# Kernel optimization log

Hardware: AMD Instinct MI355X
Metric: run time of the kernel (lower is better)

## Reference

```python
import jax, jax.numpy as jnp
import numpy as np

K = 20  # top-K neighbors per stock
SLOPE = 0.2  # LeakyReLU negative slope


def _gru_layer(x, Wih, Whh, bih, bhh):
    # x: [N, T, D]; PyTorch GRU gate order: r, z, n
    H = Whh.shape[1]
    def step(h, xt):
        gi = xt @ Wih.T + bih            # [N, 3H]
        gh = h @ Whh.T + bhh             # [N, 3H]
        ir, iz, inn = jnp.split(gi, 3, axis=1)
        hr, hz, hn = jnp.split(gh, 3, axis=1)
        r = jax.nn.sigmoid(ir + hr)
        z = jax.nn.sigmoid(iz + hz)
        n = jnp.tanh(inn + r * hn)
        h_new = (1.0 - z) * n + z * h
        return h_new, h_new
    h0 = jnp.zeros((x.shape[0], H), x.dtype)
    _, ys = jax.lax.scan(step, h0, jnp.swapaxes(x, 0, 1))
    return jnp.swapaxes(ys, 0, 1)        # [N, T, H]


def _cos_sim(x, y):
    # torch: xy / (||x|| ||y||^T), NaN (0/0) replaced by 0
    xy = x @ y.T
    xn = jnp.sqrt(jnp.sum(x * x, axis=1, keepdims=True))
    yn = jnp.sqrt(jnp.sum(y * y, axis=1, keepdims=True))
    denom = xn @ yn.T
    safe = jnp.where(denom == 0.0, 1.0, denom)
    return jnp.where(denom == 0.0, 0.0, xy / safe)


def setup_inputs() -> dict:
    key = jax.random.key(0)
    ks = jax.random.split(key, 20)
    N, T, F, H = 4096, 64, 32, 128
    def rn(k, shape, scale=0.1):
        return jax.random.normal(k, shape, dtype=jnp.float32) * scale
    b01 = lambda n: jnp.full((n,), 0.1, jnp.float32)
    return {
        'x': jax.random.normal(ks[0], (N, T, F), dtype=jnp.float32),
        'Wih0': rn(ks[1], (3 * H, F)), 'Whh0': rn(ks[2], (3 * H, H)),
        'bih0': rn(ks[3], (3 * H,)), 'bhh0': rn(ks[4], (3 * H,)),
        'Wih1': rn(ks[5], (3 * H, H)), 'Whh1': rn(ks[6], (3 * H, H)),
        'bih1': rn(ks[7], (3 * H,)), 'bhh1': rn(ks[8], (3 * H,)),
        'W_hc': rn(ks[9], (H, H)), 'b_hc': b01(H),
        'W_hs': rn(ks[10], (H, H)), 'b_hs': b01(H),
        'W_fore': rn(ks[11], (H, H)), 'b_fore': b01(H),
        'W_back': rn(ks[12], (H, H)), 'b_back': b01(H),
        'W_indi': rn(ks[13], (H, H)), 'b_indi': b01(H),
        'W_out': rn(ks[14], (1, H)), 'b_out': b01(1),
    }


def reference(x, Wih0, Whh0, bih0, bhh0, Wih1, Whh1, bih1, bhh1,
              W_hc, b_hc, W_hs, b_hs, W_fore, b_fore, W_back, b_back,
              W_indi, b_indi, W_out, b_out):
    lrelu = lambda v: jax.nn.leaky_relu(v, SLOPE)
    h = _gru_layer(x, Wih0, Whh0, bih0, bhh0)
    h = _gru_layer(h, Wih1, Whh1, bih1, bhh1)
    g = h[:, -1, :]                                   # [N, H] last-step GRU output
    N = g.shape[0]

    sim = _cos_sim(g, g)                              # [N, N]
    diag = jnp.diagonal(sim)
    sim_off = sim * (1.0 - jnp.eye(N, dtype=sim.dtype))

    # top-K (by |sim|) neighbor mask via scatter
    cols = jax.lax.top_k(jnp.abs(sim_off), K)[1]      # [N, K]
    rows = jnp.repeat(jnp.arange(N), K)
    mask = jnp.zeros((N, N), sim.dtype).at[rows, cols.reshape(-1)].set(1.0)

    tks = sim_off * mask
    col_nz = (jnp.sum(tks, axis=0) != 0).astype(sim.dtype)
    tks = tks + jnp.diag(col_nz * diag)

    # concept features; zero rows (empty concepts) are masked instead of filtered
    concept_raw = tks.T @ g                           # [N, H]
    valid = (jnp.sum(concept_raw, axis=1) != 0).astype(g.dtype)
    cf = lrelu(concept_raw @ W_hc.T + b_hc) * valid[:, None]

    attn = jax.nn.softmax(_cos_sim(g, cf), axis=0)    # softmax over stocks per concept
    hs = lrelu((attn @ cf) @ W_hs.T + b_hs)
    back = lrelu(hs @ W_back.T + b_back)
    fore = lrelu(hs @ W_fore.T + b_fore)
    indi = lrelu((g - back) @ W_indi.T + b_indi)
    pred = (fore + indi) @ W_out.T + b_out            # [N, 1]
    return pred.squeeze(-1)
```

## Files before the change

### kernel.cpp

```cpp
#include <hip/hip_runtime.h>
#include <hip/hip_bf16.h>


typedef float f32x4 __attribute__((ext_vector_type(4)));
typedef short s16x8 __attribute__((ext_vector_type(8)));
typedef unsigned short u16;
typedef unsigned long long u64;

#define DEVFN static __device__ __forceinline__

DEVFN u16 f2bf(float f) {
  union { float f; unsigned u; } v; v.f = f;
  return (u16)((v.u + 0x7FFFu + ((v.u >> 16) & 1u)) >> 16);
}

DEVFN unsigned f2bf_pk(float lo, float hi) {
  union { __hip_bfloat162 h; unsigned u; } p;
  p.h = __float22bfloat162_rn(make_float2(lo, hi));
  return p.u;
}

DEVFN f32x4 mfma16(s16x8 a, s16x8 b, f32x4 c) {
  return __builtin_amdgcn_mfma_f32_16x16x32_bf16(a, b, c, 0, 0, 0);
}
// ... 94 lines not shown
#pragma unroll
    for (int i = 0; i < 4; i += 2) {
      float hn[2];
#pragma unroll
      for (int q = 0; q < 2; ++q) {
        int ii = i + q;
        float rr = sigmf(ai[0][ii] + brz0[0]);
        float zg = sigmf(ai[1][ii] + brz0[1]);
        float nn = tanhf_fast(ai[2][ii] + bin0 + rr * bhn0);
        hn[q] = nn - zg * nn;
        h0reg[ii] = hn[q];
      }
      unsigned pk = f2bf_pk(hn[0], hn[1]);
      int m = quad * 4 + i;
      sh_h0[0][m * 136 + c]       = (u16)pk;
      sh_h0[0][(m + 1) * 136 + c] = (u16)(pk >> 16);
    }
  }

#define GRU_STEP(T, CUR, NXT)                                                     \
  {                                                                               \
    __syncthreads();                                                              \
    s16x8 ah0[4], ah1[4];                                                         \
    _Pragma("unroll")                                                             \
    for (int kk = 0; kk < 4; ++kk) {                                              \
      ah0[kk] = *(const s16x8*)(sh_h0[CUR] + l16 * 136 + kk * 32 + quad * 8);     \
      ah1[kk] = *(const s16x8*)(sh_h1[CUR] + l16 * 136 + kk * 32 + quad * 8);     \
    }                                                                             \
    s16x8 ax = *(const s16x8*)(sh_x[(T) + 1] + l16 * 40 + quad * 8);              \
    f32x4 r1a, z1a, ni1, nh1, r0a, z0a, ni0, nh0;                                 \
    r1a = mfma16(ah0[0], B1ih[0][0], zz4);                                        \
    z1a = mfma16(ah0[0], B1ih[1][0], zz4);                                        \
    ni1 = mfma16(ah0[0], B1ih[2][0], zz4);                                        \
    nh1 = mfma16(ah1[0], B1hh[2][0], zz4);                                        \
    r0a = mfma16(ax, B0ih[0], zz4);                                               \
    z0a = mfma16(ax, B0ih[1], zz4);                                               \
    ni0 = mfma16(ax, B0ih[2], zz4);                                               \
    nh0 = mfma16(ah0[0], B0hh[2][0], zz4);                                        \
    _Pragma("unroll")                                                             \
    for (int kk = 1; kk < 4; ++kk) {                                              \
      r1a = mfma16(ah0[kk], B1ih[0][kk], r1a);                                    \
      z1a = mfma16(ah0[kk], B1ih[1][kk], z1a);                                    \
      ni1 = mfma16(ah0[kk], B1ih[2][kk], ni1);                                    \
      nh1 = mfma16(ah1[kk], B1hh[2][kk], nh1);                                    \
      nh0 = mfma16(ah0[kk], B0hh[2][kk], nh0);                                    \
    }                                                                             \
    _Pragma("unroll")                                                             \
    for (int kk = 0; kk < 4; ++kk) {                                              \
      r1a = mfma16(ah1[kk], B1hh[0][kk], r1a);                                    \
      z1a = mfma16(ah1[kk], B1hh[1][kk], z1a);                                    \
      r0a = mfma16(ah0[kk], B0hh[0][kk], r0a);                                    \
      z0a = mfma16(ah0[kk], B0hh[1][kk], z0a);                                    \
    }                                                                             \
    _Pragma("unroll")                                                             \
    for (int i = 0; i < 4; i += 2) {                                              \
      float hn[2];                                                                \
      _Pragma("unroll")                                                           \
      for (int q = 0; q < 2; ++q) {                                               \
        int ii = i + q;                                                           \
        float rr = sigmf(r1a[ii] + brz1[0]);                                      \
        float zg = sigmf(z1a[ii] + brz1[1]);                                      \
        float nn = tanhf_fast(ni1[ii] + bin1 + rr * (nh1[ii] + bhn1));            \
        hn[q] = nn + zg * (h1reg[ii] - nn);                                       \
        h1reg[ii] = hn[q];                                                        \
      }                                                                           \
      unsigned pk = f2bf_pk(hn[0], hn[1]);                                        \
      int m = quad * 4 + i;                                                       \
      sh_h1[NXT][m * 136 + c]       = (u16)pk;                                    \
      sh_h1[NXT][(m + 1) * 136 + c] = (u16)(pk >> 16);                            \
    }                                                                             \
    _Pragma("unroll")                                                             \
    for (int i = 0; i < 4; i += 2) {                                              \
      float hn[2];                                                                \
      _Pragma("unroll")                                                           \
      for (int q = 0; q < 2; ++q) {                                               \
        int ii = i + q;                                                           \
        float rr = sigmf(r0a[ii] + brz0[0]);                                      \
        float zg = sigmf(z0a[ii] + brz0[1]);                                      \
        float nn = tanhf_fast(ni0[ii] + bin0 + rr * (nh0[ii] + bhn0));            \
        hn[q] = nn + zg * (h0reg[ii] - nn);                                       \
        h0reg[ii] = hn[q];                                                        \
      }                                                                           \
      unsigned pk = f2bf_pk(hn[0], hn[1]);                                        \
      int m = quad * 4 + i;                                                       \
      sh_h0[NXT][m * 136 + c]       = (u16)pk;                                    \
      sh_h0[NXT][(m + 1) * 136 + c] = (u16)(pk >> 16);                            \
    }                                                                             \
  }

  for (int t2 = 0; t2 < 31; ++t2) {
    int t = t2 * 2;
    GRU_STEP(t, 0, 1);
    GRU_STEP(t + 1, 1, 0);
  }
  GRU_STEP(62, 0, 1);
#undef GRU_STEP

  __syncthreads();
  {
    s16x8 ah0[4], ah1[4];
#pragma unroll
    for (int kk = 0; kk < 4; ++kk) {
      ah0[kk] = *(const s16x8*)(sh_h0[1] + l16 * 136 + kk * 32 + quad * 8);
      ah1[kk] = *(const s16x8*)(sh_h1[1] + l16 * 136 + kk * 32 + quad * 8);
    }
    f32x4 r1a, z1a, ni1, nh1;
    r1a = mfma16(ah0[0], B1ih[0][0], zz4);
    z1a = mfma16(ah0[0], B1ih[1][0], zz4);
    ni1 = mfma16(ah0[0], B1ih[2][0], zz4);
    nh1 = mfma16(ah1[0], B1hh[2][0], zz4);
#pragma unroll
    for (int kk = 1; kk < 4; ++kk) {
      r1a = mfma16(ah0[kk], B1ih[0][kk], r1a);
      z1a = mfma16(ah0[kk], B1ih[1][kk], z1a);
      ni1 = mfma16(ah0[kk], B1ih[2][kk], ni1);
      nh1 = mfma16(ah1[kk], B1hh[2][kk], nh1);
    }
#pragma unroll
    for (int kk = 0; kk < 4; ++kk) {
      r1a = mfma16(ah1[kk], B1hh[0][kk], r1a);
      z1a = mfma16(ah1[kk], B1hh[1][kk], z1a);
    }
    float hv[4];
#pragma unroll
    for (int i = 0; i < 4; ++i) {
      int m = quad * 4 + i;
      float rr = sigmf(r1a[i] + brz1[0]);
      float zg = sigmf(z1a[i] + brz1[1]);
      float nn = tanhf_fast(ni1[i] + bin1 + rr * (nh1[i] + bhn1));
      float hnew = nn + zg * (h1reg[i] - nn);
      hv[i] = hnew;
      g_out[(size_t)(r0 + m) * 128 + c] = hnew;
      gbf[(size_t)(r0 + m) * 128 + c]   = f2bf(hnew);
    }
#pragma unroll
    for (int i = 0; i < 4; ++i) {
      float s = hv[i] * hv[i];
      s += __shfl_xor(s, 1);
      s += __shfl_xor(s, 2);
      s += __shfl_xor(s, 4);
      s += __shfl_xor(s, 8);
      if (l16 == 0) red16[quad * 4 + i][w] = s;
    }
  }
  __syncthreads();
  if (tid < 16) {
    float s = 0.f;
#pragma unroll
    for (int k = 0; k < 8; ++k) s += red16[tid][k];
    rn[r0 + tid] = (s == 0.f) ? 0.f : rsqrtf(s);
  }
}

template<int MODE>
__launch_bounds__(256, 1)
__global__ void cos_gemm(const u16* __restrict__ A, const u16* __restrict__ B,
                         const float* __restrict__ rnA, const float* __restrict__ rnB,
                         float* __restrict__ C, u16* __restrict__ E,
                         float* __restrict__ colsum)
{
  __shared__ u16 shA[128 * 136];
  __shared__ u16 shB[128 * 136];
  const int tid = threadIdx.x;
  const int l = tid & 63, wv = tid >> 6;
  const int quad = l >> 4, l16 = l & 15;
  const int i0 = blockIdx.y * 128, j0 = blockIdx.x * 128;
  {
    int r = tid >> 1, half = tid & 1;
    const int4* sa = (const int4*)(A + (size_t)(i0 + r) * 128 + half * 64);
    int4* da = (int4*)(shA + r * 136 + half * 64);
    const int4* sb = (const int4*)(B + (size_t)(j0 + r) * 128 + half * 64);
    int4* db = (int4*)(shB + r * 136 + half * 64);
#pragma unroll
    for (int q = 0; q < 8; ++q) { da[q] = sa[q]; db[q] = sb[q]; }
  }
  __syncthreads();
  const int wm = wv >> 1, wn = wv & 1;
  f32x4 acc[4][4];
  const f32x4 zz4 = {0.f, 0.f, 0.f, 0.f};
#pragma unroll
  for (int a = 0; a < 4; ++a)
#pragma unroll
    for (int b = 0; b < 4; ++b) acc[a][b] = zz4;
#pragma unroll
  for (int kk = 0; kk < 4; ++kk) {
    s16x8 af[4], bfr[4];
#pragma unroll
    for (int mt = 0; mt < 4; ++mt)
      af[mt] = *(const s16x8*)(shA + (wm * 64 + mt * 16 + l16) * 136 + kk * 32 + quad * 8);
#pragma unroll
    for (int nt = 0; nt < 4; ++nt)
      bfr[nt] = *(const s16x8*)(shB + (wn * 64 + nt * 16 + l16) * 136 + kk * 32 + quad * 8);
#pragma unroll
    for (int mt = 0; mt < 4; ++mt)
#pragma unroll
      for (int nt = 0; nt < 4; ++nt) acc[mt][nt] = mfma16(af[mt], bfr[nt], acc[mt][nt]);
  }
  float ra[4][4];
#pragma unroll
  for (int mt = 0; mt < 4; ++mt)
#pragma unroll
    for (int i = 0; i < 4; ++i) ra[mt][i] = rnA[i0 + wm * 64 + mt * 16 + quad * 4 + i];
#pragma unroll
  for (int nt = 0; nt < 4; ++nt) {
    int col = j0 + wn * 64 + nt * 16 + l16;
    float rb = rnB[col];
    float psum = 0.f;
#pragma unroll
    for (int mt = 0; mt < 4; ++mt)
#pragma unroll
      for (int i = 0; i < 4; ++i) {
        int row = i0 + wm * 64 + mt * 16 + quad * 4 + i;
        float v = acc[mt][nt][i] * ra[mt][i] * rb;
        if constexpr (MODE == 0) {
          C[(size_t)row * 4096 + col] = v;
        } else {
          float e = __expf(v);
          E[(size_t)row * 4096 + col] = f2bf(e);
          psum += e;
        }
      }
    if constexpr (MODE == 1) {
      psum += __shfl_xor(psum, 16);
      psum += __shfl_xor(psum, 32);
      if (quad == 0) atomicAdd(colsum + col, psum);
    }
  }
}

__launch_bounds__(256, 1)
__global__ void topk_select(const float* __restrict__ sim,
                            int* __restrict__ gselj, float* __restrict__ gselv,
                            int* __restrict__ cnt, int* __restrict__ touched)
{
  __shared__ unsigned hist[2048];
  __shared__ u64 cand[3072];
  __shared__ int selj[20];
  __shared__ unsigned ws4[4];
  __shared__ unsigned wmin4[4], wmax4[4];
  __shared__ int shb, shcnt;
  const int tid = threadIdx.x;
  const int row = blockIdx.x;
  const int l = tid & 63, wv = tid >> 6;

  for (int i = tid; i < 2048; i += 256) hist[i] = 0;
  if (tid == 0) shcnt = 0;

  unsigned key[4][4];
  unsigned lmin = 0xFFFFFFFFu, lmax = 0u;
#pragma unroll
  for (int q = 0; q < 4; ++q) {
    int e0 = (q * 256 + tid) * 4;
    float4 v = *(const float4*)(sim + (size_t)row * 4096 + e0);
    key[q][0] = (e0 + 0 == row) ? 0u : (__float_as_uint(v.x) & 0x7FFFFFFFu);
    key[q][1] = (e0 + 1 == row) ? 0u : (__float_as_uint(v.y) & 0x7FFFFFFFu);
    key[q][2] = (e0 + 2 == row) ? 0u : (__float_as_uint(v.z) & 0x7FFFFFFFu);
    key[q][3] = (e0 + 3 == row) ? 0u : (__float_as_uint(v.w) & 0x7FFFFFFFu);
#pragma unroll
    for (int c = 0; c < 4; ++c) {
      unsigned k = key[q][c];
      lmin = k < lmin ? k : lmin;
      lmax = k > lmax ? k : lmax;
    }
  }
#pragma unroll
  for (int off = 1; off < 64; off <<= 1) {
    unsigned om = __shfl_xor(lmin, off); lmin = om < lmin ? om : lmin;
    unsigned ox = __shfl_xor(lmax, off); lmax = ox > lmax ? ox : lmax;
  }
  if (l == 0) { wmin4[wv] = lmin; wmax4[wv] = lmax; }
  __syncthreads();
  const unsigned kmin = min(min(wmin4[0], wmin4[1]), min(wmin4[2], wmin4[3]));
  const unsigned kmax = max(max(wmax4[0], wmax4[1]), max(wmax4[2], wmax4[3]));
  const float binscale = (kmax > kmin) ? (2047.0f / (float)(kmax - kmin)) : 0.0f;

#define BIN_OF(k) ((int)((float)((k) - kmin) * binscale))

#pragma unroll
  for (int q = 0; q < 4; ++q)
#pragma unroll
    for (int c = 0; c < 4; ++c) {
      int bin = BIN_OF(key[q][c]); if (bin > 2047) bin = 2047;
      atomicAdd(&hist[bin], 1u);
    }
  __syncthreads();

  unsigned s = 0;
#pragma unroll
  for (int j = 0; j < 8; ++j) s += hist[tid * 8 + j];
  unsigned r = s;
#pragma unroll
  for (int off = 1; off < 64; off <<= 1) {
    unsigned o = __shfl_down(r, off);
    if (l + off < 64) r += o;
  }
  if (l == 0) ws4[wv] = r;
  __syncthreads();
  unsigned upper = 0;
  for (int q = wv + 1; q < 4; ++q) upper += ws4[q];
  unsigned excl = upper + (r - s);
  if (excl < 20u && excl + s >= 20u) {
    unsigned cum = excl;
    for (int j = 7; j >= 0; --j) {
      cum += hist[tid * 8 + j];
      if (cum >= 20u) { shb = tid * 8 + j; break; }
    }
  }
  __syncthreads();
  const int b = shb;

#pragma unroll
  for (int q = 0; q < 4; ++q) {
    int e0 = (q * 256 + tid) * 4;
#pragma unroll
    for (int c = 0; c < 4; ++c) {
      int bin = BIN_OF(key[q][c]); if (bin > 2047) bin = 2047;
      if (bin >= b) {
        int p = atomicAdd(&shcnt, 1);
        if (p < 3072) cand[p] = ((u64)key[q][c] << 32) | (u64)(4095 - (e0 + c));
      }
    }
  }
#undef BIN_OF
  __syncthreads();
  const int C = (shcnt < 3072) ? shcnt : 3072;

  if (wv == 0) {
    if (C <= 64) {
      u64 mykey = (l < C) ? cand[l] : 0ull;
      for (int it = 0; it < 20; ++it) {
        u64 m = mykey;
#pragma unroll
        for (int off = 1; off < 64; off <<= 1) {
          u64 o = __shfl_xor(m, off);
          if (o > m) m = o;
        }
        if (mykey == m) mykey = 0ull;
        if (l == 0) selj[it] = 4095 - (int)(m & 0xFFFull);
      }
    } else {
      for (int it = 0; it < 20; ++it) {
        u64 best = 0ull; int bpos = -1;
        for (int p = l; p < C; p += 64) {
          u64 cv = cand[p];
          if (cv > best) { best = cv; bpos = p; }
        }
        u64 mine = best;
#pragma unroll
        for (int off = 1; off < 64; off <<= 1) {
          u64 o = __shfl_xor(best, off);
          if (o > best) best = o;
        }
        if (mine == best && bpos >= 0 && best != 0ull) cand[bpos] = 0ull;
        if (l == 0) selj[it] = 4095 - (int)(best & 0xFFFull);
      }
    }
  }
  __syncthreads();
  if (tid < 20) {
    int idx = selj[tid];
    float sv = (idx == row) ? 0.f : sim[(size_t)row * 4096 + idx];
    gselj[row * 20 + tid] = idx;
    gselv[row * 20 + tid] = sv;
    atomicAdd(&cnt[idx], 1);
    if (sv != 0.f) atomicOr(touched + idx, 1);
  }
}

__launch_bounds__(1024, 1)
__global__ void scan4096(const int* __restrict__ cnt, int* __restrict__ offs,
                         int* __restrict__ cur)
{
  __shared__ int wsum[16];
  const int t = threadIdx.x, l = t & 63, wv = t >> 6;
  int4 c = ((const int4*)cnt)[t];
  int s = c.x + c.y + c.z + c.w;
  int ps = s;
#pragma unroll
  for (int off = 1; off < 64; off <<= 1) {
    int o = __shfl_up(ps, off);
    if (l >= off) ps += o;
  }
  if (l == 63) wsum[wv] = ps;
  __syncthreads();
  if (t == 0) {
    int a = 0;
#pragma unroll
    for (int q = 0; q < 16; ++q) { int x = wsum[q]; wsum[q] = a; a += x; }
  }
  __syncthreads();
  int base = wsum[wv] + (ps - s);
  int4 o4;
  o4.x = base; o4.y = o4.x + c.x; o4.z = o4.y + c.y; o4.w = o4.z + c.z;
  ((int4*)offs)[t] = o4;
  ((int4*)cur)[t] = o4;
}

__global__ void scatter_entries(const int* __restrict__ gselj, const float* __restrict__ gselv,
                                int* __restrict__ cur, int* __restrict__ eid,
                                float* __restrict__ ev)
{
  unsigned idx = blockIdx.x * 256 + threadIdx.x;
  unsigned row = idx / 20u;
  int j = gselj[idx]; float v = gselv[idx];
  int pos = atomicAdd(&cur[j], 1);
  eid[pos] = (int)row; ev[pos] = v;
}

__launch_bounds__(128, 1)
__global__ void concept_cf(const int* __restrict__ offs, const int* __restrict__ cnt,
                           const int* __restrict__ eid, const float* __restrict__ ev,
                           const float* __restrict__ g, const float* __restrict__ rng,
                           const int* __restrict__ touched,
                           const float* __restrict__ Whc, const float* __restrict__ bhc,
                           float* __restrict__ cf, u16* __restrict__ cfbf,
                           float* __restrict__ rncf)
{
  __shared__ float shc[128];
  __shared__ float red2[2];
  const int j = blockIdx.x, d = threadIdx.x;
  const int l = d & 63, wv = d >> 6;
  const int off = offs[j], n = cnt[j];
  float acc = 0.f;
  for (int p = 0; p < n; ++p) {
    int i = eid[off + p]; float v = ev[off + p];
    acc += v * g[(size_t)i * 128 + d];
  }
  if (touched[j] && rng[j] != 0.f) acc += g[(size_t)j * 128 + d];
  float s = acc;
#pragma unroll
  for (int o = 32; o >= 1; o >>= 1) s += __shfl_xor(s, o);
  if (l == 0) red2[wv] = s;
  shc[d] = acc;
  __syncthreads();
  float valid = ((red2[0] + red2[1]) != 0.f) ? 1.f : 0.f;
  float o = bhc[d];
  const float4* wr = (const float4*)(Whc + (size_t)d * 128);
#pragma unroll 8
  for (int q = 0; q < 32; ++q) {
    float4 w4 = wr[q];
    float4 c4 = *((const float4*)shc + q);
    o += c4.x * w4.x + c4.y * w4.y + c4.z * w4.z + c4.w * w4.w;
  }
  float cfv = lrelu(o) * valid;
  cf[(size_t)j * 128 + d] = cfv;
  cfbf[(size_t)j * 128 + d] = f2bf(cfv);
  __syncthreads();
  float nn = cfv * cfv;
#pragma unroll
  for (int of = 32; of >= 1; of >>= 1) nn += __shfl_xor(nn, of);
  if (l == 0) red2[wv] = nn;
  __syncthreads();
  if (d == 0) {
    float q2 = red2[0] + red2[1];
    rncf[j] = (q2 == 0.f) ? 0.f : rsqrtf(q2);
  }
}

__launch_bounds__(256, 1)
__global__ void scale_cfT(const float* __restrict__ cf, const float* __restrict__ colsum,
                          u16* __restrict__ cfTs)
{
  __shared__ float tile[32][132];
  __shared__ float rz[32];
  const int t = threadIdx.x;
  const int c0 = blockIdx.x * 32;
  if (t < 32) rz[t] = __builtin_amdgcn_rcpf(colsum[c0 + t]);
#pragma unroll
  for (int k = 0; k < 4; ++k) {
    int lin = k * 256 + t;
    int r = lin >> 5;
    int q = lin & 31;
    float4 v = *(const float4*)(cf + (size_t)(c0 + r) * 128 + q * 4);
    tile[r][q * 4 + 0] = v.x; tile[r][q * 4 + 1] = v.y;
    tile[r][q * 4 + 2] = v.z; tile[r][q * 4 + 3] = v.w;
  }
  __syncthreads();
#pragma unroll
  for (int k = 0; k < 4; ++k) {
    int lin = k * 256 + t;
    int n  = lin >> 3;
    int c4 = (lin & 7) * 4;
    ushort4 o;
    o.x = f2bf(tile[c4 + 0][n] * rz[c4 + 0]);
    o.y = f2bf(tile[c4 + 1][n] * rz[c4 + 1]);
    o.z = f2bf(tile[c4 + 2][n] * rz[c4 + 2]);
    o.w = f2bf(tile[c4 + 3][n] * rz[c4 + 3]);
    *(ushort4*)(cfTs + (size_t)n * 4096 + c0 + c4) = o;
  }
}

__launch_bounds__(256, 1)
__global__ void attn_cf(const u16* __restrict__ attn, const u16* __restrict__ cfT,
                        float* __restrict__ hs_pre)
{
  __shared__ u16 shw[16 * 136];
  const int tid = threadIdx.x;
  const int l = tid & 63, wv = tid >> 6;
  const int quad = l >> 4, l16 = l & 15;
  const int r0 = blockIdx.x * 16;
  f32x4 acc[2];
  const f32x4 zz4 = {0.f, 0.f, 0.f, 0.f};
  acc[0] = zz4; acc[1] = zz4;
  for (int kc = 0; kc < 32; ++kc) {
    if (kc) __syncthreads();
    {
      int r = tid >> 4, seg = tid & 15;
      *(int4*)(shw + r * 136 + seg * 8) =
        *(const int4*)(attn + (size_t)(r0 + r) * 4096 + kc * 128 + seg * 8);
    }
    __syncthreads();
#pragma unroll
    for (int kk = 0; kk < 4; ++kk) {
      s16x8 a = *(const s16x8*)(shw + l16 * 136 + kk * 32 + quad * 8);
#pragma unroll
      for (int nt = 0; nt < 2; ++nt) {
        int n = wv * 32 + nt * 16 + l16;
        s16x8 b = *(const s16x8*)(cfT + (size_t)n * 4096 + kc * 128 + kk * 32 + quad * 8);
        acc[nt] = mfma16(a, b, acc[nt]);
      }
    }
  }
#pragma unroll
  for (int nt = 0; nt < 2; ++nt)
#pragma unroll
    for (int i = 0; i < 4; ++i) {
      int row = r0 + quad * 4 + i;
      int col = wv * 32 + nt * 16 + l16;
      hs_pre[(size_t)row * 128 + col] = acc[nt][i];
    }
}

__launch_bounds__(256, 1)
__global__ void head_kernel(const float* __restrict__ hs_pre, const float* __restrict__ g,
                            const u16* __restrict__ whs, const u16* __restrict__ wfore,
                            const u16* __restrict__ wback, const u16* __restrict__ windi,
                            const float* __restrict__ b_hs, const float* __restrict__ b_fore,
                            const float* __restrict__ b_back, const float* __restrict__ b_indi,
                            const float* __restrict__ W_out, const float* __restrict__ b_out,
                            float* __restrict__ outp)
{
  __shared__ u16 bufin[16 * 136];
  __shared__ u16 bufB[16 * 136];
  __shared__ float bufF[16 * 132];
  __shared__ float shWout[128];
  const int tid = threadIdx.x;
  const int l = tid & 63, wv = tid >> 6;
  const int quad = l >> 4, l16 = l & 15;
  const int r0 = blockIdx.x * 16;
  const f32x4 zz4 = {0.f, 0.f, 0.f, 0.f};

  if (tid < 128) shWout[tid] = W_out[tid];
  for (int idx = tid; idx < 2048; idx += 256) {
    int j = idx >> 7, n = idx & 127;
    bufin[j * 136 + n] = f2bf(hs_pre[(size_t)(r0 + j) * 128 + n]);
  }
  __syncthreads();
  {
    s16x8 a[4];
#pragma unroll
    for (int kk = 0; kk < 4; ++kk)
      a[kk] = *(const s16x8*)(bufin + l16 * 136 + kk * 32 + quad * 8);
    f32x4 acc[2]; acc[0] = zz4; acc[1] = zz4;
#pragma unroll
    for (int nt = 0; nt < 2; ++nt) {
      int n = wv * 32 + nt * 16 + l16;
#pragma unroll
      for (int kk = 0; kk < 4; ++kk)
        acc[nt] = mfma16(a[kk], *(const s16x8*)(whs + n * 128 + kk * 32 + quad * 8), acc[nt]);
    }
#pragma unroll
    for (int nt = 0; nt < 2; ++nt) {
      int n = wv * 32 + nt * 16 + l16;
      float bb = b_hs[n];
#pragma unroll
      for (int i = 0; i < 4; ++i)
        bufB[(quad * 4 + i) * 136 + n] = f2bf(lrelu(acc[nt][i] + bb));
    }
  }
  __syncthreads();
  {
    s16x8 a[4];
#pragma unroll
    for (int kk = 0; kk < 4; ++kk)
      a[kk] = *(const s16x8*)(bufB + l16 * 136 + kk * 32 + quad * 8);
    f32x4 aF[2], aB[2]; aF[0] = zz4; aF[1] = zz4; aB[0] = zz4; aB[1] = zz4;
#pragma unroll
    for (int nt = 0; nt < 2; ++nt) {
      int n = wv * 32 + nt * 16 + l16;
#pragma unroll
      for (int kk = 0; kk < 4; ++kk) {
        aF[nt] = mfma16(a[kk], *(const s16x8*)(wfore + n * 128 + kk * 32 + quad * 8), aF[nt]);
        aB[nt] = mfma16(a[kk], *(const s16x8*)(wback + n * 128 + kk * 32 + quad * 8), aB[nt]);
      }
    }
#pragma unroll
    for (int nt = 0; nt < 2; ++nt) {
      int n = wv * 32 + nt * 16 + l16;
      float bf_ = b_fore[n], bb_ = b_back[n];
#pragma unroll
      for (int i = 0; i < 4; ++i) {
        int m = quad * 4 + i;
        bufF[m * 132 + n] = lrelu(aF[nt][i] + bf_);
        float back = lrelu(aB[nt][i] + bb_);
        float gv = g[(size_t)(r0 + m) * 128 + n];
        bufin[m * 136 + n] = f2bf(gv - back);
      }
    }
  }
  __syncthreads();
  {
    s16x8 a[4];
#pragma unroll
    for (int kk = 0; kk < 4; ++kk)
      a[kk] = *(const s16x8*)(bufin + l16 * 136 + kk * 32 + quad * 8);
    f32x4 acc[2]; acc[0] = zz4; acc[1] = zz4;
#pragma unroll
    for (int nt = 0; nt < 2; ++nt) {
      int n = wv * 32 + nt * 16 + l16;
#pragma unroll
      for (int kk = 0; kk < 4; ++kk)
        acc[nt] = mfma16(a[kk], *(const s16x8*)(windi + n * 128 + kk * 32 + quad * 8), acc[nt]);
    }
#pragma unroll
    for (int nt = 0; nt < 2; ++nt) {
      int n = wv * 32 + nt * 16 + l16;
      float bi_ = b_indi[n];
#pragma unroll
      for (int i = 0; i < 4; ++i)
        bufF[(quad * 4 + i) * 132 + n] += lrelu(acc[nt][i] + bi_);
    }
  }
  __syncthreads();
  if (tid < 16) {
    float s = b_out[0];
    const float* fr = bufF + tid * 132;
    for (int n = 0; n < 128; ++n) s += fr[n] * shWout[n];
    outp[r0 + tid] = s;
  }
}

static const size_t OFF_A       = 0;
static const size_t OFF_ATTN    = 67108864;
static const size_t OFF_G       = 100663296;
static const size_t OFF_GBF     = 102760448;
static const size_t OFF_RNG     = 103809024;
static const size_t OFF_SELJ    = 103825408;
static const size_t OFF_SELV    = 104153088;
static const size_t OFF_EID     = 104480768;
static const size_t OFF_EV      = 104808448;
static const size_t OFF_CNT     = 105136128;
static const size_t OFF_TOUCH   = 105152512;
static const size_t OFF_COLSUM  = 105168896;
static const size_t OFF_OFFS    = 105185280;
static const size_t OFF_CUR     = 105201664;
static const size_t OFF_CF      = 105218048;
static const size_t OFF_CFBF    = 107315200;
static const size_t OFF_CFTS    = 108363776;
static const size_t OFF_RNCF    = 109412352;
static const size_t OFF_HSPRE   = 109428736;
static const size_t OFF_WB      = 111525888;

extern "C" void kernel_launch(void* const* d_in, const int* in_sizes, int n_in,
                              void* d_out, int out_size, void* d_ws, size_t ws_size,
                              hipStream_t stream)
{
  (void)in_sizes; (void)n_in; (void)out_size; (void)ws_size;
  const float* x      = (const float*)d_in[0];
  const float* Wih0   = (const float*)d_in[1];
  const float* Whh0   = (const float*)d_in[2];
  const float* bih0   = (const float*)d_in[3];
  const float* bhh0   = (const float*)d_in[4];
  const float* Wih1   = (const float*)d_in[5];
  const float* Whh1   = (const float*)d_in[6];
  const float* bih1   = (const float*)d_in[7];
  const float* bhh1   = (const float*)d_in[8];
  const float* W_hc   = (const float*)d_in[9];
  const float* b_hc   = (const float*)d_in[10];
  const float* W_hs   = (const float*)d_in[11];
  const float* b_hs   = (const float*)d_in[12];
  const float* W_fore = (const float*)d_in[13];
  const float* b_fore = (const float*)d_in[14];
  const float* W_back = (const float*)d_in[15];
  const float* b_back = (const float*)d_in[16];
  const float* W_indi = (const float*)d_in[17];
  const float* b_indi = (const float*)d_in[18];
  const float* W_out  = (const float*)d_in[19];
  const float* b_out  = (const float*)d_in[20];

  char* ws = (char*)d_ws;
  float* simbuf  = (float*)(ws + OFF_A);
  u16*   attnb   = (u16*)(ws + OFF_ATTN);
  float* gbuf    = (float*)(ws + OFF_G);
  u16*   gbf     = (u16*)(ws + OFF_GBF);
  float* rng     = (float*)(ws + OFF_RNG);
  int*   gselj   = (int*)(ws + OFF_SELJ);
  float* gselv   = (float*)(ws + OFF_SELV);
  int*   eid     = (int*)(ws + OFF_EID);
  float* ev      = (float*)(ws + OFF_EV);
  int*   cntb    = (int*)(ws + OFF_CNT);
  int*   touched = (int*)(ws + OFF_TOUCH);
  float* colsum  = (float*)(ws + OFF_COLSUM);
  int*   offsb   = (int*)(ws + OFF_OFFS);
  int*   curb    = (int*)(ws + OFF_CUR);
  float* cf      = (float*)(ws + OFF_CF);
  u16*   cfbf    = (u16*)(ws + OFF_CFBF);
  u16*   cfTs    = (u16*)(ws + OFF_CFTS);
  float* rncf    = (float*)(ws + OFF_RNCF);
  float* hs_pre  = (float*)(ws + OFF_HSPRE);
  u16*   wsB     = (u16*)(ws + OFF_WB);
  u16 *wih0b = wsB, *whh0b = wsB + 12288, *wih1b = wsB + 61440, *whh1b = wsB + 110592;
  u16 *whsb = wsB + 159744, *wforeb = wsB + 176128, *wbackb = wsB + 192512, *windib = wsB + 208896;

  cvt_all<<<880, 256, 0, stream>>>(Wih0, Whh0, Wih1, Whh1, W_hs, W_fore, W_back, W_indi,
                                   wsB, cntb);

  gru_fused<<<256, 512, 0, stream>>>(x, wih0b, whh0b, bih0, bhh0,
                                     wih1b, whh1b, bih1, bhh1, gbuf, gbf, rng);

  cos_gemm<0><<<dim3(32, 32), 256, 0, stream>>>(gbf, gbf, rng, rng, simbuf,
                                                (u16*)nullptr, (float*)nullptr);

  topk_select<<<4096, 256, 0, stream>>>(simbuf, gselj, gselv, cntb, touched);
  scan4096<<<1, 1024, 0, stream>>>(cntb, offsb, curb);
  scatter_entries<<<320, 256, 0, stream>>>(gselj, gselv, curb, eid, ev);
  concept_cf<<<4096, 128, 0, stream>>>(offsb, cntb, eid, ev, gbuf, rng, touched,
                                       W_hc, b_hc, cf, cfbf, rncf);

  cos_gemm<1><<<dim3(32, 32), 256, 0, stream>>>(gbf, cfbf, rng, rncf, (float*)nullptr,
                                                attnb, colsum);
  scale_cfT<<<128, 256, 0, stream>>>(cf, colsum, cfTs);
  attn_cf<<<256, 256, 0, stream>>>(attnb, cfTs, hs_pre);

  head_kernel<<<256, 256, 0, stream>>>(hs_pre, gbuf, whsb, wforeb, wbackb, windib,
                                       b_hs, b_fore, b_back, b_indi, W_out, b_out,
                                       (float*)d_out);
}
```

Before: 429.3 us.

## Fuse similarity GEMM into top-k and recompute attention instead of materializing NxN

Replaces the materialized 4096x4096 fp32 similarity matrix and its separate top-k pass with a fused kernel that computes 16-row similarity tiles with MFMA three times (min/max, histogram, candidate collection), never writing the matrix to memory. Likewise the bf16 exp-attention matrix is no longer stored: one GEMM only accumulates column sums, and the attention-times-cf kernel recomputes exp(cos) per tile in shared memory. This removes roughly 100MB of global traffic at the cost of redundant matrix-core recompute and a 512-bin histogram per row instead of 2048 bins, which may produce more candidates.

```diff
diff --git a/kernel.cpp b/kernel.cpp
--- a/kernel.cpp
+++ b/kernel.cpp
@@ -270,12 +270,272 @@
   }
 }
 
-template<int MODE>
+__launch_bounds__(512, 1)
+__global__ void sim_topk(const u16* __restrict__ A, const float* __restrict__ rn,
+                         int* __restrict__ gselj, float* __restrict__ gselv,
+                         int* __restrict__ cnt, int* __restrict__ touched)
+{
+  __shared__ unsigned hist[16][512];
+  __shared__ u64 cand[16][256];
+  __shared__ unsigned kmn[16], kmx[16];
+  __shared__ int cnt16[16], bthr[16];
+  const int tid = threadIdx.x;
+  const int w = tid >> 6, l = tid & 63;
+  const int quad = l >> 4, l16 = l & 15;
+  const int r0 = blockIdx.x * 16;
+  const f32x4 zz4 = {0.f, 0.f, 0.f, 0.f};
+
+  for (int i = tid; i < 16 * 512; i += 512) (&hist[0][0])[i] = 0u;
+  if (tid < 16) { kmn[tid] = 0xFFFFFFFFu; kmx[tid] = 0u; cnt16[tid] = 0; }
+
+  s16x8 af[4];
+#pragma unroll
+  for (int kk = 0; kk < 4; ++kk)
+    af[kk] = *(const s16x8*)(A + (size_t)(r0 + l16) * 128 + kk * 32 + quad * 8);
+  float ra[4];
+#pragma unroll
+  for (int i = 0; i < 4; ++i) ra[i] = rn[r0 + quad * 4 + i];
+  __syncthreads();
+
+#define SIM_TILE(T, BODY)                                                       \
+  {                                                                             \
+    int col = (T) * 128 + w * 16 + l16;                                         \
+    s16x8 bf[4];                                                                \
+    _Pragma("unroll")                                                           \
+    for (int kk = 0; kk < 4; ++kk)                                              \
+      bf[kk] = *(const s16x8*)(A + (size_t)col * 128 + kk * 32 + quad * 8);     \
+    f32x4 acc = zz4;                                                            \
+    _Pragma("unroll")                                                           \
+    for (int kk = 0; kk < 4; ++kk) acc = mfma16(af[kk], bf[kk], acc);           \
+    float rb = rn[col];                                                         \
+    _Pragma("unroll")                                                           \
+    for (int i = 0; i < 4; ++i) {                                               \
+      float v = acc[i] * ra[i] * rb;                                            \
+      unsigned kv = (col == r0 + quad * 4 + i)                                  \
+                        ? 0u : (__float_as_uint(v) & 0x7FFFFFFFu);              \
+      BODY                                                                      \
+    }                                                                           \
+  }
+
+  unsigned lmn[4] = {0xFFFFFFFFu, 0xFFFFFFFFu, 0xFFFFFFFFu, 0xFFFFFFFFu};
+  unsigned lmx[4] = {0u, 0u, 0u, 0u};
+  for (int t = 0; t < 32; ++t)
+    SIM_TILE(t, { (void)v;
+      lmn[i] = kv < lmn[i] ? kv : lmn[i];
+      lmx[i] = kv > lmx[i] ? kv : lmx[i]; })
+#pragma unroll
+  for (int i = 0; i < 4; ++i) {
+#pragma unroll
+    for (int off = 1; off < 16; off <<= 1) {
+      unsigned om = __shfl_xor(lmn[i], off); lmn[i] = om < lmn[i] ? om : lmn[i];
+      unsigned ox = __shfl_xor(lmx[i], off); lmx[i] = ox > lmx[i] ? ox : lmx[i];
+    }
+    if (l16 == 0) {
+      atomicMin(&kmn[quad * 4 + i], lmn[i]);
+      atomicMax(&kmx[quad * 4 + i], lmx[i]);
+    }
+  }
+  __syncthreads();
+  unsigned kb[4]; float scl[4];
+#pragma unroll
+  for (int i = 0; i < 4; ++i) {
+    unsigned mn = kmn[quad * 4 + i], mx = kmx[quad * 4 + i];
+    kb[i] = mn;
+    scl[i] = (mx > mn) ? (511.0f / (float)(mx - mn)) : 0.0f;
+  }
+
+  for (int t = 0; t < 32; ++t)
+    SIM_TILE(t, { (void)v;
+      int bin = (int)((float)(kv - kb[i]) * scl[i]); if (bin > 511) bin = 511;
+      atomicAdd(&hist[quad * 4 + i][bin], 1u); })
+  __syncthreads();
+
+  for (int rr = 0; rr < 2; ++rr) {
+    int row = w * 2 + rr;
+    unsigned s = 0;
+#pragma unroll
+    for (int j = 0; j < 8; ++j) s += hist[row][l * 8 + j];
+    unsigned r = s;
+#pragma unroll
+    for (int off = 1; off < 64; off <<= 1) {
+      unsigned o = __shfl_down(r, off);
+      if (l + off < 64) r += o;
+    }
+    unsigned excl = r - s;
+    if (excl < 20u && excl + s >= 20u) {
+      unsigned cum = excl;
+      for (int j = 7; j >= 0; --j) {
+        cum += hist[row][l * 8 + j];
+        if (cum >= 20u) { bthr[row] = l * 8 + j; break; }
+      }
+    }
+  }
+  __syncthreads();
+  int bth[4];
+#pragma unroll
+  for (int i = 0; i < 4; ++i) bth[i] = bthr[quad * 4 + i];
+
+  for (int t = 0; t < 32; ++t)
+    SIM_TILE(t, {
+      int bin = (int)((float)(kv - kb[i]) * scl[i]); if (bin > 511) bin = 511;
+      if (bin >= bth[i]) {
+        int p = atomicAdd(&cnt16[quad * 4 + i], 1);
+        if (p < 256) {
+          unsigned sgn = kv ? (__float_as_uint(v) >> 31) : 0u;
+          cand[quad * 4 + i][p] =
+              ((u64)kv << 13) | ((u64)(4095 - col) << 1) | (u64)sgn;
+        }
+      }
+    })
+#undef SIM_TILE
+  __syncthreads();
+
+  for (int rr = 0; rr < 2; ++rr) {
+    int row = w * 2 + rr;
+    int C = cnt16[row] < 256 ? cnt16[row] : 256;
+    int grow = r0 + row;
+    if (C <= 64) {
+      u64 my = (l < C) ? cand[row][l] : 0ull;
+      for (int it = 0; it < 20; ++it) {
+        u64 m = my;
+#pragma unroll
+        for (int off = 1; off < 64; off <<= 1) {
+          u64 o = __shfl_xor(m, off);
+          if (o > m) m = o;
+        }
+        if (my == m) my = 0ull;
+        if (l == 0) {
+          int idx = 4095 - (int)((m >> 1) & 0xFFFull);
+          unsigned kv = (unsigned)(m >> 13);
+          float sv = kv ? __uint_as_float(((unsigned)(m & 1) << 31) | kv) : 0.0f;
+          gselj[grow * 20 + it] = idx;
+          gselv[grow * 20 + it] = sv;
+          atomicAdd(&cnt[idx], 1);
+          if (sv != 0.f) atomicOr(touched + idx, 1);
+        }
+      }
+    } else {
+      for (int it = 0; it < 20; ++it) {
+        u64 best = 0ull; int bpos = -1;
+        for (int p = l; p < C; p += 64) {
+          u64 cv = cand[row][p];
+          if (cv > best) { best = cv; bpos = p; }
+        }
+        u64 mine = best;
+#pragma unroll
+        for (int off = 1; off < 64; off <<= 1) {
+          u64 o = __shfl_xor(best, off);
+          if (o > best) best = o;
+        }
+        if (mine == best && bpos >= 0 && best != 0ull) cand[row][bpos] = 0ull;
+        if (l == 0) {
+          int idx = 4095 - (int)((best >> 1) & 0xFFFull);
+          unsigned kv = (unsigned)(best >> 13);
+          float sv = kv ? __uint_as_float(((unsigned)(best & 1) << 31) | kv) : 0.0f;
+          gselj[grow * 20 + it] = idx;
+          gselv[grow * 20 + it] = sv;
+          atomicAdd(&cnt[idx], 1);
+          if (sv != 0.f) atomicOr(touched + idx, 1);
+        }
+      }
+    }
+  }
+}
+
+__launch_bounds__(1024, 1)
+__global__ void scan4096(const int* __restrict__ cnt, int* __restrict__ offs,
+                         int* __restrict__ cur)
+{
+  __shared__ int wsum[16];
+  const int t = threadIdx.x, l = t & 63, wv = t >> 6;
+  int4 c = ((const int4*)cnt)[t];
+  int s = c.x + c.y + c.z + c.w;
+  int ps = s;
+#pragma unroll
+  for (int off = 1; off < 64; off <<= 1) {
+    int o = __shfl_up(ps, off);
+    if (l >= off) ps += o;
+  }
+  if (l == 63) wsum[wv] = ps;
+  __syncthreads();
+  if (t == 0) {
+    int a = 0;
+#pragma unroll
+    for (int q = 0; q < 16; ++q) { int x = wsum[q]; wsum[q] = a; a += x; }
+  }
+  __syncthreads();
+  int base = wsum[wv] + (ps - s);
+  int4 o4;
+  o4.x = base; o4.y = o4.x + c.x; o4.z = o4.y + c.y; o4.w = o4.z + c.z;
+  ((int4*)offs)[t] = o4;
+  ((int4*)cur)[t] = o4;
+}
+
+__global__ void scatter_entries(const int* __restrict__ gselj, const float* __restrict__ gselv,
+                                int* __restrict__ cur, int* __restrict__ eid,
+                                float* __restrict__ ev)
+{
+  unsigned idx = blockIdx.x * 256 + threadIdx.x;
+  unsigned row = idx / 20u;
+  int j = gselj[idx]; float v = gselv[idx];
+  int pos = atomicAdd(&cur[j], 1);
+  eid[pos] = (int)row; ev[pos] = v;
+}
+
+__launch_bounds__(128, 1)
+__global__ void concept_cf(const int* __restrict__ offs, const int* __restrict__ cnt,
+                           const int* __restrict__ eid, const float* __restrict__ ev,
+                           const float* __restrict__ g, const float* __restrict__ rng,
+                           const int* __restrict__ touched,
+                           const float* __restrict__ Whc, const float* __restrict__ bhc,
+                           float* __restrict__ cf, u16* __restrict__ cfbf,
+                           float* __restrict__ rncf)
+{
+  __shared__ float shc[128];
+  __shared__ float red2[2];
+  const int j = blockIdx.x, d = threadIdx.x;
+  const int l = d & 63, wv = d >> 6;
+  const int off = offs[j], n = cnt[j];
+  float acc = 0.f;
+  for (int p = 0; p < n; ++p) {
+    int i = eid[off + p]; float v = ev[off + p];
+    acc += v * g[(size_t)i * 128 + d];
+  }
+  if (touched[j] && rng[j] != 0.f) acc += g[(size_t)j * 128 + d];
+  float s = acc;
+#pragma unroll
+  for (int o = 32; o >= 1; o >>= 1) s += __shfl_xor(s, o);
+  if (l == 0) red2[wv] = s;
+  shc[d] = acc;
+  __syncthreads();
+  float valid = ((red2[0] + red2[1]) != 0.f) ? 1.f : 0.f;
+  float o = bhc[d];
+  const float4* wr = (const float4*)(Whc + (size_t)d * 128);
+#pragma unroll 8
+  for (int q = 0; q < 32; ++q) {
+    float4 w4 = wr[q];
+    float4 c4 = *((const float4*)shc + q);
+    o += c4.x * w4.x + c4.y * w4.y + c4.z * w4.z + c4.w * w4.w;
+  }
+  float cfv = lrelu(o) * valid;
+  cf[(size_t)j * 128 + d] = cfv;
+  cfbf[(size_t)j * 128 + d] = f2bf(cfv);
+  __syncthreads();
+  float nn = cfv * cfv;
+#pragma unroll
+  for (int of = 32; of >= 1; of >>= 1) nn += __shfl_xor(nn, of);
+  if (l == 0) red2[wv] = nn;
+  __syncthreads();
+  if (d == 0) {
+    float q2 = red2[0] + red2[1];
+    rncf[j] = (q2 == 0.f) ? 0.f : rsqrtf(q2);
+  }
+}
+
 __launch_bounds__(256, 1)
-__global__ void cos_gemm(const u16* __restrict__ A, const u16* __restrict__ B,
-                         const float* __restrict__ rnA, const float* __restrict__ rnB,
-                         float* __restrict__ C, u16* __restrict__ E,
-                         float* __restrict__ colsum)
+__global__ void colsum_gemm(const u16* __restrict__ A, const u16* __restrict__ B,
+                            const float* __restrict__ rnA, const float* __restrict__ rnB,
+                            float* __restrict__ colsum)
 {
   __shared__ u16 shA[128 * 136];
   __shared__ u16 shB[128 * 136];
@@ -328,250 +588,12 @@
     for (int mt = 0; mt < 4; ++mt)
 #pragma unroll
       for (int i = 0; i < 4; ++i) {
-        int row = i0 + wm * 64 + mt * 16 + quad * 4 + i;
         float v = acc[mt][nt][i] * ra[mt][i] * rb;
-        if constexpr (MODE == 0) {
-          C[(size_t)row * 4096 + col] = v;
-        } else {
-          float e = __expf(v);
-          E[(size_t)row * 4096 + col] = f2bf(e);
-          psum += e;
-        }
-      }
-    if constexpr (MODE == 1) {
-      psum += __shfl_xor(psum, 16);
-      psum += __shfl_xor(psum, 32);
-      if (quad == 0) atomicAdd(colsum + col, psum);
-    }
-  }
-}
-
-__launch_bounds__(256, 1)
-__global__ void topk_select(const float* __restrict__ sim,
-                            int* __restrict__ gselj, float* __restrict__ gselv,
-                            int* __restrict__ cnt, int* __restrict__ touched)
-{
-  __shared__ unsigned hist[2048];
-  __shared__ u64 cand[3072];
-  __shared__ int selj[20];
-  __shared__ unsigned ws4[4];
-  __shared__ unsigned wmin4[4], wmax4[4];
-  __shared__ int shb, shcnt;
-  const int tid = threadIdx.x;
-  const int row = blockIdx.x;
-  const int l = tid & 63, wv = tid >> 6;
-
-  for (int i = tid; i < 2048; i += 256) hist[i] = 0;
-  if (tid == 0) shcnt = 0;
-
-  unsigned key[4][4];
-  unsigned lmin = 0xFFFFFFFFu, lmax = 0u;
-#pragma unroll
-  for (int q = 0; q < 4; ++q) {
-    int e0 = (q * 256 + tid) * 4;
-    float4 v = *(const float4*)(sim + (size_t)row * 4096 + e0);
-    key[q][0] = (e0 + 0 == row) ? 0u : (__float_as_uint(v.x) & 0x7FFFFFFFu);
-    key[q][1] = (e0 + 1 == row) ? 0u : (__float_as_uint(v.y) & 0x7FFFFFFFu);
-    key[q][2] = (e0 + 2 == row) ? 0u : (__float_as_uint(v.z) & 0x7FFFFFFFu);
-    key[q][3] = (e0 + 3 == row) ? 0u : (__float_as_uint(v.w) & 0x7FFFFFFFu);
-#pragma unroll
-    for (int c = 0; c < 4; ++c) {
-      unsigned k = key[q][c];
-      lmin = k < lmin ? k : lmin;
-      lmax = k > lmax ? k : lmax;
-    }
-  }
-#pragma unroll
-  for (int off = 1; off < 64; off <<= 1) {
-    unsigned om = __shfl_xor(lmin, off); lmin = om < lmin ? om : lmin;
-    unsigned ox = __shfl_xor(lmax, off); lmax = ox > lmax ? ox : lmax;
-  }
-  if (l == 0) { wmin4[wv] = lmin; wmax4[wv] = lmax; }
-  __syncthreads();
-  const unsigned kmin = min(min(wmin4[0], wmin4[1]), min(wmin4[2], wmin4[3]));
-  const unsigned kmax = max(max(wmax4[0], wmax4[1]), max(wmax4[2], wmax4[3]));
-  const float binscale = (kmax > kmin) ? (2047.0f / (float)(kmax - kmin)) : 0.0f;
-
-#define BIN_OF(k) ((int)((float)((k) - kmin) * binscale))
-
-#pragma unroll
-  for (int q = 0; q < 4; ++q)
-#pragma unroll
-    for (int c = 0; c < 4; ++c) {
-      int bin = BIN_OF(key[q][c]); if (bin > 2047) bin = 2047;
-      atomicAdd(&hist[bin], 1u);
-    }
-  __syncthreads();
-
-  unsigned s = 0;
-#pragma unroll
-  for (int j = 0; j < 8; ++j) s += hist[tid * 8 + j];
-  unsigned r = s;
-#pragma unroll
-  for (int off = 1; off < 64; off <<= 1) {
-    unsigned o = __shfl_down(r, off);
-    if (l + off < 64) r += o;
-  }
-  if (l == 0) ws4[wv] = r;
-  __syncthreads();
-  unsigned upper = 0;
-  for (int q = wv + 1; q < 4; ++q) upper += ws4[q];
-  unsigned excl = upper + (r - s);
-  if (excl < 20u && excl + s >= 20u) {
-    unsigned cum = excl;
-    for (int j = 7; j >= 0; --j) {
-      cum += hist[tid * 8 + j];
-      if (cum >= 20u) { shb = tid * 8 + j; break; }
-    }
-  }
-  __syncthreads();
-  const int b = shb;
-
-#pragma unroll
-  for (int q = 0; q < 4; ++q) {
-    int e0 = (q * 256 + tid) * 4;
-#pragma unroll
-    for (int c = 0; c < 4; ++c) {
-      int bin = BIN_OF(key[q][c]); if (bin > 2047) bin = 2047;
-      if (bin >= b) {
-        int p = atomicAdd(&shcnt, 1);
-        if (p < 3072) cand[p] = ((u64)key[q][c] << 32) | (u64)(4095 - (e0 + c));
-      }
-    }
-  }
-#undef BIN_OF
-  __syncthreads();
-  const int C = (shcnt < 3072) ? shcnt : 3072;
-
-  if (wv == 0) {
-    if (C <= 64) {
-      u64 mykey = (l < C) ? cand[l] : 0ull;
-      for (int it = 0; it < 20; ++it) {
-        u64 m = mykey;
-#pragma unroll
-        for (int off = 1; off < 64; off <<= 1) {
-          u64 o = __shfl_xor(m, off);
-          if (o > m) m = o;
-        }
-        if (mykey == m) mykey = 0ull;
-        if (l == 0) selj[it] = 4095 - (int)(m & 0xFFFull);
-      }
-    } else {
-      for (int it = 0; it < 20; ++it) {
-        u64 best = 0ull; int bpos = -1;
-        for (int p = l; p < C; p += 64) {
-          u64 cv = cand[p];
-          if (cv > best) { best = cv; bpos = p; }
-        }
-        u64 mine = best;
-#pragma unroll
-        for (int off = 1; off < 64; off <<= 1) {
-          u64 o = __shfl_xor(best, off);
-          if (o > best) best = o;
-        }
-        if (mine == best && bpos >= 0 && best != 0ull) cand[bpos] = 0ull;
-        if (l == 0) selj[it] = 4095 - (int)(best & 0xFFFull);
-      }
-    }
-  }
-  __syncthreads();
-  if (tid < 20) {
-    int idx = selj[tid];
-    float sv = (idx == row) ? 0.f : sim[(size_t)row * 4096 + idx];
-    gselj[row * 20 + tid] = idx;
-    gselv[row * 20 + tid] = sv;
-    atomicAdd(&cnt[idx], 1);
-    if (sv != 0.f) atomicOr(touched + idx, 1);
-  }
-}
-
-__launch_bounds__(1024, 1)
-__global__ void scan4096(const int* __restrict__ cnt, int* __restrict__ offs,
-                         int* __restrict__ cur)
-{
-  __shared__ int wsum[16];
-  const int t = threadIdx.x, l = t & 63, wv = t >> 6;
-  int4 c = ((const int4*)cnt)[t];
-  int s = c.x + c.y + c.z + c.w;
-  int ps = s;
-#pragma unroll
-  for (int off = 1; off < 64; off <<= 1) {
-    int o = __shfl_up(ps, off);
-    if (l >= off) ps += o;
-  }
-  if (l == 63) wsum[wv] = ps;
-  __syncthreads();
-  if (t == 0) {
-    int a = 0;
-#pragma unroll
-    for (int q = 0; q < 16; ++q) { int x = wsum[q]; wsum[q] = a; a += x; }
-  }
-  __syncthreads();
-  int base = wsum[wv] + (ps - s);
-  int4 o4;
-  o4.x = base; o4.y = o4.x + c.x; o4.z = o4.y + c.y; o4.w = o4.z + c.z;
-  ((int4*)offs)[t] = o4;
-  ((int4*)cur)[t] = o4;
-}
-
-__global__ void scatter_entries(const int* __restrict__ gselj, const float* __restrict__ gselv,
-                                int* __restrict__ cur, int* __restrict__ eid,
-                                float* __restrict__ ev)
-{
-  unsigned idx = blockIdx.x * 256 + threadIdx.x;
-  unsigned row = idx / 20u;
-  int j = gselj[idx]; float v = gselv[idx];
-  int pos = atomicAdd(&cur[j], 1);
-  eid[pos] = (int)row; ev[pos] = v;
-}
-
-__launch_bounds__(128, 1)
-__global__ void concept_cf(const int* __restrict__ offs, const int* __restrict__ cnt,
-                           const int* __restrict__ eid, const float* __restrict__ ev,
-                           const float* __restrict__ g, const float* __restrict__ rng,
-                           const int* __restrict__ touched,
-                           const float* __restrict__ Whc, const float* __restrict__ bhc,
-                           float* __restrict__ cf, u16* __restrict__ cfbf,
-                           float* __restrict__ rncf)
-{
-  __shared__ float shc[128];
-  __shared__ float red2[2];
-  const int j = blockIdx.x, d = threadIdx.x;
-  const int l = d & 63, wv = d >> 6;
-  const int off = offs[j], n = cnt[j];
-  float acc = 0.f;
-  for (int p = 0; p < n; ++p) {
-    int i = eid[off + p]; float v = ev[off + p];
-    acc += v * g[(size_t)i * 128 + d];
-  }
-  if (touched[j] && rng[j] != 0.f) acc += g[(size_t)j * 128 + d];
-  float s = acc;
-#pragma unroll
-  for (int o = 32; o >= 1; o >>= 1) s += __shfl_xor(s, o);
-  if (l == 0) red2[wv] = s;
-  shc[d] = acc;
-  __syncthreads();
-  float valid = ((red2[0] + red2[1]) != 0.f) ? 1.f : 0.f;
-  float o = bhc[d];
-  const float4* wr = (const float4*)(Whc + (size_t)d * 128);
-#pragma unroll 8
-  for (int q = 0; q < 32; ++q) {
-    float4 w4 = wr[q];
-    float4 c4 = *((const float4*)shc + q);
-    o += c4.x * w4.x + c4.y * w4.y + c4.z * w4.z + c4.w * w4.w;
-  }
-  float cfv = lrelu(o) * valid;
-  cf[(size_t)j * 128 + d] = cfv;
-  cfbf[(size_t)j * 128 + d] = f2bf(cfv);
-  __syncthreads();
-  float nn = cfv * cfv;
-#pragma unroll
-  for (int of = 32; of >= 1; of >>= 1) nn += __shfl_xor(nn, of);
-  if (l == 0) red2[wv] = nn;
-  __syncthreads();
-  if (d == 0) {
-    float q2 = red2[0] + red2[1];
-    rncf[j] = (q2 == 0.f) ? 0.f : rsqrtf(q2);
+        psum += __expf(v);
+      }
+    psum += __shfl_xor(psum, 16);
+    psum += __shfl_xor(psum, 32);
+    if (quad == 0) atomicAdd(colsum + col, psum);
   }
 }
 
@@ -609,32 +631,57 @@
 }
 
 __launch_bounds__(256, 1)
-__global__ void attn_cf(const u16* __restrict__ attn, const u16* __restrict__ cfT,
-                        float* __restrict__ hs_pre)
-{
-  __shared__ u16 shw[16 * 136];
+__global__ void attn_fused(const u16* __restrict__ gbf, const float* __restrict__ rng,
+                           const u16* __restrict__ cfbf, const float* __restrict__ rncf,
+                           const u16* __restrict__ cfT, float* __restrict__ hs_pre)
+{
+  __shared__ u16 shE[16 * 136];
   const int tid = threadIdx.x;
   const int l = tid & 63, wv = tid >> 6;
   const int quad = l >> 4, l16 = l & 15;
   const int r0 = blockIdx.x * 16;
-  f32x4 acc[2];
   const f32x4 zz4 = {0.f, 0.f, 0.f, 0.f};
-  acc[0] = zz4; acc[1] = zz4;
-  for (int kc = 0; kc < 32; ++kc) {
-    if (kc) __syncthreads();
-    {
-      int r = tid >> 4, seg = tid & 15;
-      *(int4*)(shw + r * 136 + seg * 8) =
-        *(const int4*)(attn + (size_t)(r0 + r) * 4096 + kc * 128 + seg * 8);
+
+  s16x8 ag[4];
+#pragma unroll
+  for (int kk = 0; kk < 4; ++kk)
+    ag[kk] = *(const s16x8*)(gbf + (size_t)(r0 + l16) * 128 + kk * 32 + quad * 8);
+  float ra[4];
+#pragma unroll
+  for (int i = 0; i < 4; ++i) ra[i] = rng[r0 + quad * 4 + i];
+
+  f32x4 acc[2]; acc[0] = zz4; acc[1] = zz4;
+  for (int ct = 0; ct < 32; ++ct) {
+    int c0 = ct * 128;
+    f32x4 a2[2]; a2[0] = zz4; a2[1] = zz4;
+#pragma unroll
+    for (int nt = 0; nt < 2; ++nt) {
+      int cc = c0 + wv * 32 + nt * 16 + l16;
+#pragma unroll
+      for (int kk = 0; kk < 4; ++kk) {
+        s16x8 b = *(const s16x8*)(cfbf + (size_t)cc * 128 + kk * 32 + quad * 8);
+        a2[nt] = mfma16(ag[kk], b, a2[nt]);
+      }
+    }
+    if (ct) __syncthreads();
+#pragma unroll
+    for (int nt = 0; nt < 2; ++nt) {
+      int cl = wv * 32 + nt * 16 + l16;
+      float rb = rncf[c0 + cl];
+#pragma unroll
+      for (int i = 0; i < 4; ++i) {
+        float e = __expf(a2[nt][i] * ra[i] * rb);
+        shE[(quad * 4 + i) * 136 + cl] = f2bf(e);
+      }
     }
     __syncthreads();
 #pragma unroll
     for (int kk = 0; kk < 4; ++kk) {
-      s16x8 a = *(const s16x8*)(shw + l16 * 136 + kk * 32 + quad * 8);
+      s16x8 a = *(const s16x8*)(shE + l16 * 136 + kk * 32 + quad * 8);
 #pragma unroll
       for (int nt = 0; nt < 2; ++nt) {
         int n = wv * 32 + nt * 16 + l16;
-        s16x8 b = *(const s16x8*)(cfT + (size_t)n * 4096 + kc * 128 + kk * 32 + quad * 8);
+        s16x8 b = *(const s16x8*)(cfT + (size_t)n * 4096 + c0 + kk * 32 + quad * 8);
         acc[nt] = mfma16(a, b, acc[nt]);
       }
     }
@@ -758,26 +805,24 @@
   }
 }
 
-static const size_t OFF_A       = 0;
-static const size_t OFF_ATTN    = 67108864;
-static const size_t OFF_G       = 100663296;
-static const size_t OFF_GBF     = 102760448;
-static const size_t OFF_RNG     = 103809024;
-static const size_t OFF_SELJ    = 103825408;
-static const size_t OFF_SELV    = 104153088;
-static const size_t OFF_EID     = 104480768;
-static const size_t OFF_EV      = 104808448;
-static const size_t OFF_CNT     = 105136128;
-static const size_t OFF_TOUCH   = 105152512;
-static const size_t OFF_COLSUM  = 105168896;
-static const size_t OFF_OFFS    = 105185280;
-static const size_t OFF_CUR     = 105201664;
-static const size_t OFF_CF      = 105218048;
-static const size_t OFF_CFBF    = 107315200;
-static const size_t OFF_CFTS    = 108363776;
-static const size_t OFF_RNCF    = 109412352;
-static const size_t OFF_HSPRE   = 109428736;
-static const size_t OFF_WB      = 111525888;
+static const size_t OFF_G      = 0;
+static const size_t OFF_GBF    = 2097152;
+static const size_t OFF_RNG    = 3145728;
+static const size_t OFF_SELJ   = 3162112;
+static const size_t OFF_SELV   = 3489792;
+static const size_t OFF_EID    = 3817472;
+static const size_t OFF_EV     = 4145152;
+static const size_t OFF_CNT    = 4472832;
+static const size_t OFF_TOUCH  = 4489216;
+static const size_t OFF_COLSUM = 4505600;
+static const size_t OFF_OFFS   = 4521984;
+static const size_t OFF_CUR    = 4538368;
+static const size_t OFF_CF     = 4554752;
+static const size_t OFF_CFBF   = 6651904;
+static const size_t OFF_CFTS   = 7700480;
+static const size_t OFF_RNCF   = 8749056;
+static const size_t OFF_HSPRE  = 8765440;
+static const size_t OFF_WB     = 10862592;
 
 extern "C" void kernel_launch(void* const* d_in, const int* in_sizes, int n_in,
                               void* d_out, int out_size, void* d_ws, size_t ws_size,
@@ -807,8 +852,6 @@
   const float* b_out  = (const float*)d_in[20];
 
   char* ws = (char*)d_ws;
-  float* simbuf  = (float*)(ws + OFF_A);
-  u16*   attnb   = (u16*)(ws + OFF_ATTN);
   float* gbuf    = (float*)(ws + OFF_G);
   u16*   gbf     = (u16*)(ws + OFF_GBF);
   float* rng     = (float*)(ws + OFF_RNG);
@@ -836,19 +879,16 @@
   gru_fused<<<256, 512, 0, stream>>>(x, wih0b, whh0b, bih0, bhh0,
                                      wih1b, whh1b, bih1, bhh1, gbuf, gbf, rng);
 
-  cos_gemm<0><<<dim3(32, 32), 256, 0, stream>>>(gbf, gbf, rng, rng, simbuf,
-                                                (u16*)nullptr, (float*)nullptr);
-
-  topk_select<<<4096, 256, 0, stream>>>(simbuf, gselj, gselv, cntb, touched);
+  sim_topk<<<256, 512, 0, stream>>>(gbf, rng, gselj, gselv, cntb, touched);
+
   scan4096<<<1, 1024, 0, stream>>>(cntb, offsb, curb);
   scatter_entries<<<320, 256, 0, stream>>>(gselj, gselv, curb, eid, ev);
   concept_cf<<<4096, 128, 0, stream>>>(offsb, cntb, eid, ev, gbuf, rng, touched,
                                        W_hc, b_hc, cf, cfbf, rncf);
 
-  cos_gemm<1><<<dim3(32, 32), 256, 0, stream>>>(gbf, cfbf, rng, rncf, (float*)nullptr,
-                                                attnb, colsum);
+  colsum_gemm<<<dim3(32, 32), 256, 0, stream>>>(gbf, cfbf, rng, rncf, colsum);
   scale_cfT<<<128, 256, 0, stream>>>(cf, colsum, cfTs);
-  attn_cf<<<256, 256, 0, stream>>>(attnb, cfTs, hs_pre);
+  attn_fused<<<256, 256, 0, stream>>>(gbf, rng, cfbf, rncf, cfTs, hs_pre);
 
   head_kernel<<<256, 256, 0, stream>>>(hs_pre, gbuf, whsb, wforeb, wbackb, windib,
                                        b_hs, b_fore, b_back, b_indi, W_out, b_out,
```

Measured after the change: 504.7 us. 1.18x slower.
